# Optimization experiments

Measured on AMD Instinct MI355X. Metric: run time of the kernel, lower is better.

The kernel has to match this reference:

```python
import jax, jax.numpy as jnp
import numpy as np


def setup_inputs() -> dict:
    key = jax.random.key(0)
    k1, k2 = jax.random.split(key)
    emb_in = jax.random.normal(k1, (2048, 32), dtype=jnp.float32)
    sum_weights = jax.random.normal(k2, (2048,), dtype=jnp.float32)
    return {"emb_in": emb_in, "sum_weights": sum_weights}


def reference(emb_in, sum_weights):
    # emb_in: [n, f], sum_weights: [n]
    n, f = emb_in.shape
    # a[k] = emb_in[k // n]  (each row repeated n times consecutively)
    a = jnp.repeat(emb_in, n, axis=0)          # [n*n, f]
    # b[k] = emb_in[k % n]   (whole tensor tiled n times)
    b = jnp.tile(emb_in, (n, 1))               # [n*n, f]
    # weights column matches b: w[k] = sum_weights[k % n]
    w = jnp.tile(sum_weights[:, None], (n, 1)) # [n*n, 1]
    sample = jnp.concatenate((a, b, w), axis=1)  # [n*n, 2*f + 1]
    return sample
```

## Files before the change

### kernel.cpp

```cpp
#include <hip/hip_runtime.h>


#define NROWS 2048u
#define BLOCK_ROWS 512u
#define WAVE_ROWS 128u
#define SLAB_ROWS 16u
#define NSLABS 8u
#define SLAB_FLOATS (SLAB_ROWS * 65u)
#define SLAB_F4 (SLAB_FLOATS / 4u)
#define LDS_BYTES 61440u

typedef float f32x4 __attribute__((ext_vector_type(4)));

__global__ __launch_bounds__(256) void expand_pipe(
    const float* __restrict__ emb,
    const float* __restrict__ sw,
    f32x4* __restrict__ out)
{
    extern __shared__ __align__(16) float dynlds[];

    const unsigned tid  = threadIdx.x;
    const unsigned wave = tid >> 6;
    const unsigned lane = tid & 63u;

    const unsigned r0 = blockIdx.x * BLOCK_ROWS + wave * WAVE_ROWS;
    const unsigned i  = r0 >> 11;
    const unsigned j0 = r0 & (NROWS - 1u);

    float* buf0 = dynlds + (wave * 2u + 0u) * SLAB_FLOATS;
    float* buf1 = dynlds + (wave * 2u + 1u) * SLAB_FLOATS;

    const float vi = emb[i * 32u + (lane & 31u)];
    const unsigned rbase = (lane >> 5) * 8u;
#pragma unroll
    for (unsigned rp = 0; rp < 8u; ++rp) {
        buf0[(rbase + rp) * 65u + (lane & 31u)] = vi;
        buf1[(rbase + rp) * 65u + (lane & 31u)] = vi;
    }

    const unsigned d0 = (lane >> 3) * 65u + 32u + (lane & 7u) * 4u;

    {
        const f32x4* ej = (const f32x4*)(emb + (size_t)j0 * 32u);
        const f32x4 pa = ej[lane];
        const f32x4 pb = ej[lane + 64u];
        const float ps = sw[j0 + (lane & 15u)];
        buf0[d0 + 0u] = pa.x; buf0[d0 + 1u] = pa.y;
        buf0[d0 + 2u] = pa.z; buf0[d0 + 3u] = pa.w;
        buf0[d0 + 520u + 0u] = pb.x; buf0[d0 + 520u + 1u] = pb.y;
        buf0[d0 + 520u + 2u] = pb.z; buf0[d0 + 520u + 3u] = pb.w;
        if (lane < 16u) buf0[lane * 65u + 64u] = ps;
    }

#pragma unroll
    for (unsigned s = 0; s < NSLABS; ++s) {
        float* CUR = (s & 1u) ? buf1 : buf0;
        float* NXT = (s & 1u) ? buf0 : buf1;

        f32x4 pa, pb;
        float ps = 0.0f;
        if (s + 1u < NSLABS) {
            const f32x4* ej =
                (const f32x4*)(emb + (size_t)(j0 + (s + 1u) * SLAB_ROWS) * 32u);
            pa = ej[lane];
            pb = ej[lane + 64u];
            ps = sw[j0 + (s + 1u) * SLAB_ROWS + (lane & 15u)];
        }

        const f32x4* L4 = (const f32x4*)CUR;
        const unsigned obase = ((r0 + s * SLAB_ROWS) >> 4) * SLAB_F4;
#pragma unroll
        for (unsigned p = 0; p < 4u; ++p)
            out[obase + p * 64u + lane] = L4[p * 64u + lane];
        if (lane < 4u)
            out[obase + 256u + lane] = L4[256u + lane];

        if (s + 1u < NSLABS) {
            NXT[d0 + 0u] = pa.x; NXT[d0 + 1u] = pa.y;
            NXT[d0 + 2u] = pa.z; NXT[d0 + 3u] = pa.w;
            NXT[d0 + 520u + 0u] = pb.x; NXT[d0 + 520u + 1u] = pb.y;
            NXT[d0 + 520u + 2u] = pb.z; NXT[d0 + 520u + 3u] = pb.w;
            if (lane < 16u) NXT[lane * 65u + 64u] = ps;
        }
    }
}

extern "C" void kernel_launch(void* const* d_in, const int* in_sizes, int n_in,
                              void* d_out, int out_size, void* d_ws, size_t ws_size,
                              hipStream_t stream) {
    const float* emb = (const float*)d_in[0];
    const float* sw  = (const float*)d_in[1];
    f32x4* out       = (f32x4*)d_out;

    const unsigned blocks = (NROWS * NROWS) / BLOCK_ROWS;
    expand_pipe<<<dim3(blocks), dim3(256), LDS_BYTES, stream>>>(emb, sw, out);
}
```

Before: 202.6 us.

## Convert expand kernel to persistent grid looping over sixteen tiles per block

Replaces the 8192-block launch with 512 persistent blocks, each looping over 16 tiles. Each wave keeps the same j-range of emb rows and steps i by 128, so the b-slab pattern repeats across tiles. The next tile's i row is prefetched and rewritten into the LDS buffers during the slab pipeline. The aim is to cut block launch and prologue overhead. The cost is fewer resident waves to hide store latency, and output is written with a large stride between tiles.

Result: no change. 204.4 us (+0.9%).

```diff
diff --git a/kernel.cpp b/kernel.cpp
--- a/kernel.cpp
+++ b/kernel.cpp
@@ -2,17 +2,16 @@
 
 
 #define NROWS 2048u
-#define BLOCK_ROWS 512u
-#define WAVE_ROWS 128u
 #define SLAB_ROWS 16u
-#define NSLABS 8u
 #define SLAB_FLOATS (SLAB_ROWS * 65u)
 #define SLAB_F4 (SLAB_FLOATS / 4u)
+#define NBLOCKS 512u
+#define NTILES 16u
 #define LDS_BYTES 61440u
 
 typedef float f32x4 __attribute__((ext_vector_type(4)));
 
-__global__ __launch_bounds__(256) void expand_pipe(
+__global__ __launch_bounds__(256) void expand_persist(
     const float* __restrict__ emb,
     const float* __restrict__ sw,
     f32x4* __restrict__ out)
@@ -22,24 +21,23 @@
     const unsigned tid  = threadIdx.x;
     const unsigned wave = tid >> 6;
     const unsigned lane = tid & 63u;
+    const unsigned b    = blockIdx.x;
 
-    const unsigned r0 = blockIdx.x * BLOCK_ROWS + wave * WAVE_ROWS;
-    const unsigned i  = r0 >> 11;
-    const unsigned j0 = r0 & (NROWS - 1u);
+    const unsigned j0 = (b & 3u) * 512u + wave * 128u;
+    const unsigned i0 = (b * 4u + wave) >> 4;
+    const unsigned c     = lane & 31u;
+    const unsigned rbase = (lane >> 5) * 8u;
+    const unsigned d0 = (lane >> 3) * 65u + 32u + (lane & 7u) * 4u;
 
-    float* buf0 = dynlds + (wave * 2u + 0u) * SLAB_FLOATS;
-    float* buf1 = dynlds + (wave * 2u + 1u) * SLAB_FLOATS;
+    float* buf0 = dynlds + (wave * 2u) * SLAB_FLOATS;
+    float* buf1 = buf0 + SLAB_FLOATS;
 
-    const float vi = emb[i * 32u + (lane & 31u)];
-    const unsigned rbase = (lane >> 5) * 8u;
+    float vi = emb[i0 * 32u + c];
 #pragma unroll
     for (unsigned rp = 0; rp < 8u; ++rp) {
-        buf0[(rbase + rp) * 65u + (lane & 31u)] = vi;
-        buf1[(rbase + rp) * 65u + (lane & 31u)] = vi;
+        buf0[(rbase + rp) * 65u + c] = vi;
+        buf1[(rbase + rp) * 65u + c] = vi;
     }
-
-    const unsigned d0 = (lane >> 3) * 65u + 32u + (lane & 7u) * 4u;
-
     {
         const f32x4* ej = (const f32x4*)(emb + (size_t)j0 * 32u);
         const f32x4 pa = ej[lane];
@@ -47,41 +45,59 @@
         const float ps = sw[j0 + (lane & 15u)];
         buf0[d0 + 0u] = pa.x; buf0[d0 + 1u] = pa.y;
         buf0[d0 + 2u] = pa.z; buf0[d0 + 3u] = pa.w;
-        buf0[d0 + 520u + 0u] = pb.x; buf0[d0 + 520u + 1u] = pb.y;
-        buf0[d0 + 520u + 2u] = pb.z; buf0[d0 + 520u + 3u] = pb.w;
+        buf0[d0 + 520u] = pb.x; buf0[d0 + 521u] = pb.y;
+        buf0[d0 + 522u] = pb.z; buf0[d0 + 523u] = pb.w;
         if (lane < 16u) buf0[lane * 65u + 64u] = ps;
     }
 
+    float viN = 0.0f;
+#pragma unroll 1
+    for (unsigned k = 0; k < NTILES; ++k) {
+        const unsigned tb32 = (b + 512u * k) * 32u + wave * 8u;
 #pragma unroll
-    for (unsigned s = 0; s < NSLABS; ++s) {
-        float* CUR = (s & 1u) ? buf1 : buf0;
-        float* NXT = (s & 1u) ? buf0 : buf1;
+        for (unsigned s = 0; s < 8u; ++s) {
+            float* CUR = (s & 1u) ? buf1 : buf0;
+            float* NXT = (s & 1u) ? buf0 : buf1;
+            const bool last = (k == NTILES - 1u) && (s == 7u);
 
-        f32x4 pa, pb;
-        float ps = 0.0f;
-        if (s + 1u < NSLABS) {
-            const f32x4* ej =
-                (const f32x4*)(emb + (size_t)(j0 + (s + 1u) * SLAB_ROWS) * 32u);
-            pa = ej[lane];
-            pb = ej[lane + 64u];
-            ps = sw[j0 + (s + 1u) * SLAB_ROWS + (lane & 15u)];
+            f32x4 pa, pb;
+            float ps = 0.0f;
+            if (!last) {
+                const unsigned jn = j0 + ((s + 1u) & 7u) * SLAB_ROWS;
+                const f32x4* ej = (const f32x4*)(emb + (size_t)jn * 32u);
+                pa = ej[lane];
+                pb = ej[lane + 64u];
+                ps = sw[jn + (lane & 15u)];
+            }
+            if (s == 6u && k + 1u < NTILES)
+                viN = emb[(i0 + (k + 1u) * 128u) * 32u + c];
+
+            const f32x4* L4 = (const f32x4*)CUR;
+            const unsigned ob = (tb32 + s) * SLAB_F4;
+#pragma unroll
+            for (unsigned p = 0; p < 4u; ++p)
+                out[ob + p * 64u + lane] = L4[p * 64u + lane];
+            if (lane < 4u)
+                out[ob + 256u + lane] = L4[256u + lane];
+
+            if (!last) {
+                NXT[d0 + 0u] = pa.x; NXT[d0 + 1u] = pa.y;
+                NXT[d0 + 2u] = pa.z; NXT[d0 + 3u] = pa.w;
+                NXT[d0 + 520u] = pb.x; NXT[d0 + 521u] = pb.y;
+                NXT[d0 + 522u] = pb.z; NXT[d0 + 523u] = pb.w;
+                if (lane < 16u) NXT[lane * 65u + 64u] = ps;
+                if (s == 7u) {
+#pragma unroll
+                    for (unsigned rp = 0; rp < 8u; ++rp)
+                        NXT[(rbase + rp) * 65u + c] = viN;
+                } else if (s == 0u) {
+#pragma unroll
+                    for (unsigned rp = 0; rp < 8u; ++rp)
+                        NXT[(rbase + rp) * 65u + c] = vi;
+                }
+            }
         }
-
-        const f32x4* L4 = (const f32x4*)CUR;
-        const unsigned obase = ((r0 + s * SLAB_ROWS) >> 4) * SLAB_F4;
-#pragma unroll
-        for (unsigned p = 0; p < 4u; ++p)
-            out[obase + p * 64u + lane] = L4[p * 64u + lane];
-        if (lane < 4u)
-            out[obase + 256u + lane] = L4[256u + lane];
-
-        if (s + 1u < NSLABS) {
-            NXT[d0 + 0u] = pa.x; NXT[d0 + 1u] = pa.y;
-            NXT[d0 + 2u] = pa.z; NXT[d0 + 3u] = pa.w;
-            NXT[d0 + 520u + 0u] = pb.x; NXT[d0 + 520u + 1u] = pb.y;
-            NXT[d0 + 520u + 2u] = pb.z; NXT[d0 + 520u + 3u] = pb.w;
-            if (lane < 16u) NXT[lane * 65u + 64u] = ps;
-        }
+        vi = viN;
     }
 }
 
@@ -92,6 +108,5 @@
     const float* sw  = (const float*)d_in[1];
     f32x4* out       = (f32x4*)d_out;
 
-    const unsigned blocks = (NROWS * NROWS) / BLOCK_ROWS;
-    expand_pipe<<<dim3(blocks), dim3(256), LDS_BYTES, stream>>>(emb, sw, out);
+    expand_persist<<<dim3(NBLOCKS), dim3(256), LDS_BYTES, stream>>>(emb, sw, out);
 }
```
